# Kernel tuning notes

Measured on AMD Instinct MI355X. Metric: run time of the kernel, lower is better.

The kernel has to match this reference:

```python
import jax, jax.numpy as jnp
import numpy as np

B, N0, N1, N2, HS, NCLS = 16384, 57, 20, 10, 5, 17
EPS = 1e-4  # SPDRectified eigenvalue floor
_TRI = np.triu_indices(HS)  # upper-tri vectorization indices


def _bilinear(x, W):
    # SPDTransform: W^T X W, W: (in, out) column-orthonormal (Stiefel)
    return jnp.einsum('ji,bjk,kl->bil', W, x, W)


def _rectify(x):
    # SPDRectified: eigh, clamp eigenvalues at EPS, recompose
    w, v = jnp.linalg.eigh(x)
    w = jnp.maximum(w, EPS)
    return jnp.einsum('bij,bj,bkj->bik', v, w, v)


def _logmap(x):
    # SPDTangentSpace log map: eigh, log eigenvalues, recompose
    w, v = jnp.linalg.eigh(x)
    w = jnp.log(w)
    return jnp.einsum('bij,bj,bkj->bik', v, w, v)


def setup_inputs() -> dict:
    key = jax.random.key(0)
    ks = jax.random.split(key, 6)
    A = jax.random.normal(ks[0], (B, N0, N0), dtype=jnp.float32)
    # SPD input: A A^T / N0 + 0.01 I
    x = jnp.einsum('bij,bkj->bik', A, A) / N0 + 0.01 * jnp.eye(N0, dtype=jnp.float32)

    def stiefel(k, m, n):
        q, _ = jnp.linalg.qr(jax.random.normal(k, (m, n), dtype=jnp.float32))
        return q  # (m, n) column-orthonormal

    W1 = stiefel(ks[1], N0, N1)
    W2 = stiefel(ks[2], N1, N2)
    W3 = stiefel(ks[3], N2, HS)
    tri = HS * (HS + 1) // 2
    lin_w = jax.random.normal(ks[4], (NCLS, tri), dtype=jnp.float32) / np.sqrt(tri)
    lin_b = jax.random.normal(ks[5], (NCLS,), dtype=jnp.float32) * 0.01
    return {"x": x, "W1": W1, "W2": W2, "W3": W3, "lin_w": lin_w, "lin_b": lin_b}


def reference(x, W1, W2, W3, lin_w, lin_b):
    x = _rectify(_bilinear(x, W1))   # [B,20,20]
    x = _rectify(_bilinear(x, W2))   # [B,10,10]
    x = _rectify(_bilinear(x, W3))   # [B,HS,HS]
    x = _logmap(x)                   # tangent space
    vec = x[:, _TRI[0], _TRI[1]]     # [B, HS*(HS+1)/2]
    return vec @ lin_w.T + lin_b     # [B, 17]
```

## Files before the change

### kernel.cpp

```cpp
#include <hip/hip_runtime.h>
#include <math.h>

#define BATCH 16384
#define N0 57
#define NX 3249
#define HS 5
#define NCLS 17
#define NTRI 15
#define EPSV 1e-4f

template<int CTRL>
__device__ __forceinline__ float dpp_mov0(float x) {
    return __int_as_float(__builtin_amdgcn_update_dpp(
        0, __float_as_int(x), CTRL, 0xF, 0xF, true));
}
__device__ __forceinline__ float wave_sum64(float x) {
    x += dpp_mov0<0x111>(x);
    x += dpp_mov0<0x112>(x);
    x += dpp_mov0<0x114>(x);
    x += dpp_mov0<0x118>(x);
    x += dpp_mov0<0x142>(x);
    x += dpp_mov0<0x143>(x);
    return x;
}

__device__ __forceinline__ float frcp(float x)  { return __builtin_amdgcn_rcpf(x); }
__device__ __forceinline__ float frsq(float x)  { return __builtin_amdgcn_rsqf(x); }
__device__ __forceinline__ float fsqrt(float x) { return __builtin_amdgcn_sqrtf(x); }

__global__ __launch_bounds__(256) void k_main(const float* __restrict__ x,
                                              const float* __restrict__ W1,
                                              const float* __restrict__ W2,
                                              const float* __restrict__ W3,
                                              float* __restrict__ y_out) {
    __shared__ float w23[100];
    __shared__ float wcs[N0 * 8];
    const int tid  = threadIdx.x;
    const int lane = tid & 63;
    const int wave = tid >> 6;
    const int m    = blockIdx.x * 4 + wave;

    if (tid < 100) {
        int k = tid / 5, j = tid % 5;
        float acc = 0.f;
        #pragma unroll
        for (int l = 0; l < 10; ++l) acc = fmaf(W2[k * 10 + l], W3[l * 5 + j], acc);
        w23[tid] = acc;
    }
    __syncthreads();
    if (tid < N0) {
        #pragma unroll
        for (int j = 0; j < 5; ++j) {
            float acc = 0.f;
            #pragma unroll
            for (int k = 0; k < 20; ++k) acc = fmaf(W1[tid * 20 + k], w23[k * 5 + j], acc);
            wcs[tid * 8 + j] = acc;
        }
    }
    __syncthreads();

    float wv[HS];
    {
        int a = (lane < N0) ? lane : 0;
        #pragma unroll
        for (int i = 0; i < HS; ++i) wv[i] = wcs[a * 8 + i];
        if (lane >= N0) { wv[0] = wv[1] = wv[2] = wv[3] = wv[4] = 0.f; }
    }

    const float* mbase = x + (size_t)m * NX;
    float s1[HS] = {0.f, 0.f, 0.f, 0.f, 0.f};
    #pragma unroll
    for (int b = 0; b < N0; ++b) {
        const int idx = (lane <= b) ? lane : b;
        float xv = mbase[b * N0 + idx];
        xv = (lane <= b) ? xv : 0.f;
        #pragma unroll
        for (int j = 0; j < HS; ++j) s1[j] = fmaf(xv, wcs[b * 8 + j], s1[j]);
    }
    const int ld = (lane < N0) ? lane : 56;
    const float xd = mbase[ld * N0 + ld];

    float p[NTRI];
    int u = 0;
    #pragma unroll
    for (int i = 0; i < HS; ++i)
        #pragma unroll
        for (int j = i; j < HS; ++j) {
            float v = fmaf(wv[i], s1[j], wv[j] * s1[i]) - xd * wv[i] * wv[j];
            p[u] = wave_sum64(v);
            ++u;
        }

    if (lane == 63) {
        float4* o = (float4*)&y_out[(size_t)m * 16];
        o[0] = make_float4(p[0],  p[1],  p[2],  p[3]);
        o[1] = make_float4(p[4],  p[5],  p[6],  p[7]);
        o[2] = make_float4(p[8],  p[9],  p[10], p[11]);
        o[3] = make_float4(p[12], p[13], p[14], 0.f);
    }
}

__global__ __launch_bounds__(64) void k_eig(const float* __restrict__ y_in,
                                            const float* __restrict__ lin_w,
                                            const float* __restrict__ lin_b,
                                            float* __restrict__ out) {
    int m = blockIdx.x * 64 + threadIdx.x;
    const float4* yin = (const float4*)&y_in[(size_t)m * 16];
    float4 q0 = yin[0], q1 = yin[1], q2 = yin[2], q3 = yin[3];
    float tri[16] = {q0.x, q0.y, q0.z, q0.w, q1.x, q1.y, q1.z, q1.w,
                     q2.x, q2.y, q2.z, q2.w, q3.x, q3.y, q3.z, q3.w};

    float A[HS][HS], V[HS][HS];
    int t = 0;
    #pragma unroll
    for (int i = 0; i < HS; ++i)
        #pragma unroll
        for (int j = i; j < HS; ++j) { A[i][j] = tri[t]; A[j][i] = tri[t]; ++t; }
    #pragma unroll
    for (int i = 0; i < HS; ++i)
        #pragma unroll
        for (int j = 0; j < HS; ++j) V[i][j] = (i == j) ? 1.f : 0.f;

    #pragma unroll
    for (int sweep = 0; sweep < 5; ++sweep) {
        #pragma unroll
        for (int p = 0; p < HS - 1; ++p) {
            #pragma unroll
            for (int q = p + 1; q < HS; ++q) {
                float apq = A[p][q];
                float app = A[p][p], aqq = A[q][q];
                bool nz = fabsf(apq) > 1e-30f;
                float theta = (aqq - app) * 0.5f * frcp(apq);
                float tt = frcp(fabsf(theta) + fsqrt(fmaf(theta, theta, 1.f)));
                tt = copysignf(tt, theta);
                tt = nz ? tt : 0.f;
                float c = frsq(fmaf(tt, tt, 1.f));
                float sn = tt * c;
                #pragma unroll
                for (int k = 0; k < HS; ++k) {
                    float akp = A[k][p], akq = A[k][q];
                    A[k][p] = fmaf(c, akp, -sn * akq);
                    A[k][q] = fmaf(sn, akp,  c * akq);
                }
                #pragma unroll
                for (int k = 0; k < HS; ++k) {
                    float apk = A[p][k], aqk = A[q][k];
                    A[p][k] = fmaf(c, apk, -sn * aqk);
                    A[q][k] = fmaf(sn, apk,  c * aqk);
                }
                #pragma unroll
                for (int k = 0; k < HS; ++k) {
                    float vkp = V[k][p], vkq = V[k][q];
                    V[k][p] = fmaf(c, vkp, -sn * vkq);
                    V[k][q] = fmaf(sn, vkp,  c * vkq);
                }
            }
        }
    }

    float lwv[HS];
    #pragma unroll
    for (int i = 0; i < HS; ++i)
        lwv[i] = 0.69314718056f * __log2f(fmaxf(A[i][i], EPSV));

    float tri2[NTRI];
    t = 0;
    #pragma unroll
    for (int i = 0; i < HS; ++i) {
        float vi[HS];
        #pragma unroll
        for (int k = 0; k < HS; ++k) vi[k] = V[i][k] * lwv[k];
        #pragma unroll
        for (int j = i; j < HS; ++j) {
            float acc = 0.f;
            #pragma unroll
            for (int k = 0; k < HS; ++k) acc = fmaf(vi[k], V[j][k], acc);
            tri2[t++] = acc;
        }
    }

    #pragma unroll
    for (int c = 0; c < NCLS; ++c) {
        float acc = lin_b[c];
        #pragma unroll
        for (int k = 0; k < NTRI; ++k) acc = fmaf(tri2[k], lin_w[c * NTRI + k], acc);
        out[(size_t)m * NCLS + c] = acc;
    }
}

extern "C" void kernel_launch(void* const* d_in, const int* in_sizes, int n_in,
                              void* d_out, int out_size, void* d_ws, size_t ws_size,
                              hipStream_t stream) {
    const float* x     = (const float*)d_in[0];
    const float* W1    = (const float*)d_in[1];
    const float* W2    = (const float*)d_in[2];
    const float* W3    = (const float*)d_in[3];
    const float* lin_w = (const float*)d_in[4];
    const float* lin_b = (const float*)d_in[5];
    float* out = (float*)d_out;
    float* y   = (float*)d_ws;

    k_main<<<BATCH / 4, 256, 0, stream>>>(x, W1, W2, W3, y);
    k_eig<<<BATCH / 64, 64, 0, stream>>>(y, lin_w, lin_b, out);
}
```

Before: 54.70 us.

## Stream full SPD matrix with float4 loads instead of triangular scalar reads

The projection kernel no longer reads the lower triangle row by row with per-lane scalar loads plus a diagonal correction. It now streams the whole 57x57 matrix as flat float4 chunks, 228 floats per iteration, with each lane keeping partial sums for four element positions. The combined weight table is split into float4 and scalar shared arrays so it can be read with vector LDS loads. The cost is reading the full matrix instead of roughly half, plus extra registers and some redundant loads in the inactive lanes, in exchange for far fewer load instructions and fully coalesced access.

```diff
diff --git a/kernel.cpp b/kernel.cpp
--- a/kernel.cpp
+++ b/kernel.cpp
@@ -33,8 +33,9 @@
                                               const float* __restrict__ W2,
                                               const float* __restrict__ W3,
                                               float* __restrict__ y_out) {
-    __shared__ float w23[100];
-    __shared__ float wcs[N0 * 8];
+    __shared__ float  w23[100];
+    __shared__ float4 wcs4[N0];
+    __shared__ float  wcs1[N0];
     const int tid  = threadIdx.x;
     const int lane = tid & 63;
     const int wave = tid >> 6;
@@ -49,36 +50,75 @@
     }
     __syncthreads();
     if (tid < N0) {
+        float r[5];
         #pragma unroll
         for (int j = 0; j < 5; ++j) {
             float acc = 0.f;
             #pragma unroll
             for (int k = 0; k < 20; ++k) acc = fmaf(W1[tid * 20 + k], w23[k * 5 + j], acc);
-            wcs[tid * 8 + j] = acc;
-        }
+            r[j] = acc;
+        }
+        wcs4[tid] = make_float4(r[0], r[1], r[2], r[3]);
+        wcs1[tid] = r[4];
     }
     __syncthreads();
 
-    float wv[HS];
+    const bool act = lane < N0;
+    const int  e0  = 4 * lane;
+    int col[4], r0[4];
+    #pragma unroll
+    for (int c = 0; c < 4; ++c) {
+        int ec = e0 + c;
+        r0[c]  = ec / N0;
+        col[c] = ec - r0[c] * N0;
+    }
+    float wv4[4][HS];
+    #pragma unroll
+    for (int c = 0; c < 4; ++c) {
+        float4 t4 = wcs4[col[c]]; float t1 = wcs1[col[c]];
+        wv4[c][0] = act ? t4.x : 0.f;  wv4[c][1] = act ? t4.y : 0.f;
+        wv4[c][2] = act ? t4.z : 0.f;  wv4[c][3] = act ? t4.w : 0.f;
+        wv4[c][4] = act ? t1   : 0.f;
+    }
+    float wva[HS];
     {
-        int a = (lane < N0) ? lane : 0;
-        #pragma unroll
-        for (int i = 0; i < HS; ++i) wv[i] = wcs[a * 8 + i];
-        if (lane >= N0) { wv[0] = wv[1] = wv[2] = wv[3] = wv[4] = 0.f; }
-    }
-
-    const float* mbase = x + (size_t)m * NX;
-    float s1[HS] = {0.f, 0.f, 0.f, 0.f, 0.f};
-    #pragma unroll
-    for (int b = 0; b < N0; ++b) {
-        const int idx = (lane <= b) ? lane : b;
-        float xv = mbase[b * N0 + idx];
-        xv = (lane <= b) ? xv : 0.f;
-        #pragma unroll
-        for (int j = 0; j < HS; ++j) s1[j] = fmaf(xv, wcs[b * 8 + j], s1[j]);
-    }
-    const int ld = (lane < N0) ? lane : 56;
-    const float xd = mbase[ld * N0 + ld];
+        int a = act ? lane : 0;
+        float4 t4 = wcs4[a]; float t1 = wcs1[a];
+        wva[0] = act ? t4.x : 0.f;  wva[1] = act ? t4.y : 0.f;
+        wva[2] = act ? t4.z : 0.f;  wva[3] = act ? t4.w : 0.f;
+        wva[4] = act ? t1   : 0.f;
+    }
+
+    const float* mb = x + (size_t)m * NX;
+    float s4[4][HS];
+    #pragma unroll
+    for (int c = 0; c < 4; ++c)
+        #pragma unroll
+        for (int j = 0; j < HS; ++j) s4[c][j] = 0.f;
+
+    #pragma unroll
+    for (int it = 0; it < 14; ++it) {
+        float4 xq = *(const float4*)(mb + 228 * it + e0);
+        float xe[4] = {xq.x, xq.y, xq.z, xq.w};
+        #pragma unroll
+        for (int c = 0; c < 4; ++c) {
+            int rc = 4 * it + r0[c];
+            float4 w4 = wcs4[rc]; float w1 = wcs1[rc];
+            s4[c][0] = fmaf(xe[c], w4.x, s4[c][0]);
+            s4[c][1] = fmaf(xe[c], w4.y, s4[c][1]);
+            s4[c][2] = fmaf(xe[c], w4.z, s4[c][2]);
+            s4[c][3] = fmaf(xe[c], w4.w, s4[c][3]);
+            s4[c][4] = fmaf(xe[c], w1,   s4[c][4]);
+        }
+    }
+
+    float st[HS];
+    {
+        float xv = mb[3192 + (act ? lane : 56)];
+        float4 w4 = wcs4[56]; float w1 = wcs1[56];
+        st[0] = xv * w4.x; st[1] = xv * w4.y; st[2] = xv * w4.z;
+        st[3] = xv * w4.w; st[4] = xv * w1;
+    }
 
     float p[NTRI];
     int u = 0;
@@ -86,7 +126,9 @@
     for (int i = 0; i < HS; ++i)
         #pragma unroll
         for (int j = i; j < HS; ++j) {
-            float v = fmaf(wv[i], s1[j], wv[j] * s1[i]) - xd * wv[i] * wv[j];
+            float v = wva[i] * st[j];
+            #pragma unroll
+            for (int c = 0; c < 4; ++c) v = fmaf(wv4[c][i], s4[c][j], v);
             p[u] = wave_sum64(v);
             ++u;
         }
```

Result: faster. 52.45 us (-4.1%).
